# Optimization experiments

Hardware: AMD Instinct MI355X
Metric: run time of the kernel (lower is better)

Reference implementation:

```python
import jax, jax.numpy as jnp
import numpy as np

D_MODEL, D_K, D_FF, N = 1024, 128, 4096, 8192

def _linear_params(key, fan_in, fan_out):
    # mimic torch nn.Linear default init (uniform +/- 1/sqrt(fan_in))
    k1, k2 = jax.random.split(key)
    bound = 1.0 / np.sqrt(fan_in)
    W = jax.random.uniform(k1, (fan_out, fan_in), jnp.float32, -bound, bound)
    b = jax.random.uniform(k2, (fan_out,), jnp.float32, -bound, bound)
    return W, b

def setup_inputs() -> dict:
    key = jax.random.key(0)
    ks = jax.random.split(key, 7)
    x = jax.random.normal(ks[0], (N, D_MODEL), jnp.float32)
    Wq, bq = _linear_params(ks[1], D_MODEL, D_K)
    Wk, bk = _linear_params(ks[2], D_MODEL, D_K)
    Wv, bv = _linear_params(ks[3], D_MODEL, D_K)
    Wp, bp = _linear_params(ks[4], D_K, D_MODEL)
    W1, b1 = _linear_params(ks[5], D_MODEL, D_FF)
    W2, b2 = _linear_params(ks[6], D_FF, D_MODEL)
    return {"x": x, "Wq": Wq, "bq": bq, "Wk": Wk, "bk": bk, "Wv": Wv, "bv": bv,
            "Wp": Wp, "bp": bp, "W1": W1, "b1": b1, "W2": W2, "b2": b2}

def reference(x, Wq, bq, Wk, bk, Wv, bv, Wp, bp, W1, b1, W2, b2):
    # projections (torch Linear: x @ W.T + b)
    Q = x @ Wq.T + bq            # [n, d_k]
    K = x @ Wk.T + bk            # [n, d_k]
    V = x @ Wv.T + bv            # [n, d_k]
    # linear attention, original evaluation order: (Q @ K^T) @ V
    attn = Q @ K.T               # [n, n]
    context = attn @ V           # [n, d_k]
    out = context @ Wp.T + bp    # [n, d_model]
    x = x + out                  # residual 1
    h = jax.nn.relu(x @ W1.T + b1)  # [n, d_ff]
    return x + (h @ W2.T + b2)   # residual 2
```

## Files before the change

kernel.cpp:

```cpp
#include <hip/hip_runtime.h>


#define MROWS 8192
#define DMODEL 1024
#define DK 128
#define DFF 4096

typedef __attribute__((ext_vector_type(8))) __bf16 bf16x8;
typedef __attribute__((ext_vector_type(4))) float f32x4;

#define BAR()     __builtin_amdgcn_s_barrier()
#define WAITV(n)  asm volatile("s_waitcnt vmcnt(" #n ")" ::: "memory")
#define LGKMC(n)  asm volatile("s_waitcnt lgkmcnt(" #n ")" ::: "memory")
#define SCHED0()  __builtin_amdgcn_sched_barrier(0)
#define GLOAD(src, dst) __builtin_amdgcn_global_load_lds( \
    (const __attribute__((address_space(1))) void*)(src), \
    (__attribute__((address_space(3))) void*)(dst), 16, 0, 0)

#define LDSO(p) ((unsigned)(unsigned long long) \
    (__attribute__((address_space(3))) const char*)(const char*)(p))

__device__ __forceinline__ bf16x8 ldsr(unsigned off) {
    bf16x8 r;
    asm volatile("ds_read_b128 %0, %1" : "=v"(r) : "v"(off));
    return r;
}

__global__ __launch_bounds__(256) void cast_f32_bf16(
    const float* __restrict__ src, __bf16* __restrict__ dst, int n8)
{
    for (int i = blockIdx.x * blockDim.x + threadIdx.x; i < n8;
         i += gridDim.x * blockDim.x) {
        const float4 a = reinterpret_cast<const float4*>(src)[2 * i];
        const float4 b = reinterpret_cast<const float4*>(src)[2 * i + 1];
        bf16x8 o;
        o[0] = (__bf16)a.x; o[1] = (__bf16)a.y; o[2] = (__bf16)a.z; o[3] = (__bf16)a.w;
        o[4] = (__bf16)b.x; o[5] = (__bf16)b.y; o[6] = (__bf16)b.z; o[7] = (__bf16)b.w;
        reinterpret_cast<bf16x8*>(dst)[i] = o;
    }
}

__device__ __forceinline__ void cast_one(const float* s, __bf16* d, int i) {
    const float4 a = reinterpret_cast<const float4*>(s)[2 * i];
    const float4 b = reinterpret_cast<const float4*>(s)[2 * i + 1];
    bf16x8 o;
    o[0] = (__bf16)a.x; o[1] = (__bf16)a.y; o[2] = (__bf16)a.z; o[3] = (__bf16)a.w;
    o[4] = (__bf16)b.x; o[5] = (__bf16)b.y; o[6] = (__bf16)b.z; o[7] = (__bf16)b.w;
    reinterpret_cast<bf16x8*>(d)[i] = o;
}

__global__ __launch_bounds__(256) void cast6(
    const float* __restrict__ s0, __bf16* __restrict__ d0,
    const float* __restrict__ s1, __bf16* __restrict__ d1,
    const float* __restrict__ s2, __bf16* __restrict__ d2,
    const float* __restrict__ s3, __bf16* __restrict__ d3,
    const float* __restrict__ s4, __bf16* __restrict__ d4,
    const float* __restrict__ s5, __bf16* __restrict__ d5)
{
    const int b = blockIdx.x, t = threadIdx.x;
    if      (b <  64)  cast_one(s0, d0, b * 256 + t);
    else if (b < 128)  cast_one(s1, d1, (b - 64) * 256 + t);
    else if (b < 192)  cast_one(s2, d2, (b - 128) * 256 + t);
    else if (b < 256)  cast_one(s3, d3, (b - 192) * 256 + t);
    else if (b < 2304) cast_one(s4, d4, (b - 256) * 256 + t);
    else               cast_one(s5, d5, (b - 2304) * 256 + t);
}

__global__ void pack_bias3(const float* __restrict__ a, const float* __restrict__ b,
                           const float* __restrict__ c, float* __restrict__ o)
{
    const int t = threadIdx.x;
    o[t] = a[t]; o[128 + t] = b[t]; o[256 + t] = c[t];
}

__global__ __launch_bounds__(256) void ffn2_reduce(
    float* __restrict__ y, const __bf16* __restrict__ P0,
    const __bf16* __restrict__ P1, const float* __restrict__ b2, int n8)
{
    for (int i = blockIdx.x * blockDim.x + threadIdx.x; i < n8;
         i += gridDim.x * blockDim.x) {
        const int col0 = (i << 3) & (DMODEL - 1);
        const float4 ba = *reinterpret_cast<const float4*>(&b2[col0]);
        const float4 bb = *reinterpret_cast<const float4*>(&b2[col0 + 4]);
        float4 o0 = reinterpret_cast<const float4*>(y)[2 * i];
        float4 o1 = reinterpret_cast<const float4*>(y)[2 * i + 1];
        const bf16x8 p0 = reinterpret_cast<const bf16x8*>(P0)[i];
        const bf16x8 p1 = reinterpret_cast<const bf16x8*>(P1)[i];
        o0.x += (float)p0[0] + (float)p1[0] + ba.x;
        o0.y += (float)p0[1] + (float)p1[1] + ba.y;
        o0.z += (float)p0[2] + (float)p1[2] + ba.z;
        o0.w += (float)p0[3] + (float)p1[3] + ba.w;
        o1.x += (float)p0[4] + (float)p1[4] + bb.x;
        o1.y += (float)p0[5] + (float)p1[5] + bb.y;
        o1.z += (float)p0[6] + (float)p1[6] + bb.z;
        o1.w += (float)p0[7] + (float)p1[7] + bb.w;
        reinterpret_cast<float4*>(y)[2 * i]     = o0;
        reinterpret_cast<float4*>(y)[2 * i + 1] = o1;
    }
}

template<bool RELU, bool RESID, bool BIAS, bool OUTBF, bool DUAL>
__global__ __launch_bounds__(256) void gemm128(
    const __bf16* __restrict__ A, int lda,
    const __bf16* __restrict__ W,
    const float* __restrict__ bias,
    const float* __restrict__ resid,
    void* __restrict__ Cout, __bf16* __restrict__ Cbf, int ldc, int K)
{
    constexpr int BK = 32;
    __shared__ __bf16 As[128 * BK];
    __shared__ __bf16 Bs[128 * BK];

    const int tid  = threadIdx.x;
    const int lane = tid & 63;
    const int w    = tid >> 6;
    const int wm   = w >> 1;
    const int wn   = w & 1;
    const int fr   = lane & 15;
    const int fq   = lane >> 4;

    const long row0 = (long)blockIdx.y * 128;
    const long col0 = (long)blockIdx.x * 128;

    const int sr = (w << 4) + (lane >> 2);
    const int sc = (lane & 3) << 3;

    const __bf16* gA0 = A + (row0 + sr) * (long)lda + sc;
    const __bf16* gA1 = A + (row0 + 64 + sr) * (long)lda + sc;
    const __bf16* gW0 = W + (col0 + sr) * (long)K + sc;
    const __bf16* gW1 = W + (col0 + 64 + sr) * (long)K + sc;

    __bf16* lA0 = &As[(w << 4) * BK];
    __bf16* lA1 = &As[((w << 4) + 64) * BK];
    __bf16* lB0 = &Bs[(w << 4) * BK];
    __bf16* lB1 = &Bs[((w << 4) + 64) * BK];

    f32x4 acc[4][4] = {};

    for (int k0 = 0; k0 < K; k0 += BK) {
        GLOAD(gA0 + k0, lA0);
        GLOAD(gA1 + k0, lA1);
        GLOAD(gW0 + k0, lB0);
        GLOAD(gW1 + k0, lB1);
        __syncthreads();

        bf16x8 af[4], bfr[4];
        #pragma unroll
        for (int m = 0; m < 4; m++)
            af[m] = *reinterpret_cast<const bf16x8*>(
                &As[(wm * 64 + m * 16 + fr) * BK + fq * 8]);
        #pragma unroll
        for (int n = 0; n < 4; n++)
            bfr[n] = *reinterpret_cast<const bf16x8*>(
                &Bs[(wn * 64 + n * 16 + fr) * BK + fq * 8]);

        #pragma unroll
        for (int m = 0; m < 4; m++)
            #pragma unroll
            for (int n = 0; n < 4; n++)
                acc[m][n] = __builtin_amdgcn_mfma_f32_16x16x32_bf16(
                    af[m], bfr[n], acc[m][n], 0, 0, 0);
        __syncthreads();
    }

    float bc[4];
    #pragma unroll
    for (int n = 0; n < 4; n++)
        bc[n] = BIAS ? bias[col0 + wn * 64 + n * 16 + fr] : 0.0f;
    #pragma unroll
    for (int m = 0; m < 4; m++) {
        #pragma unroll
        for (int j = 0; j < 4; j++) {
            const long r = row0 + wm * 64 + m * 16 + fq * 4 + j;
            #pragma unroll
            for (int n = 0; n < 4; n++) {
                const long c = col0 + wn * 64 + n * 16 + fr;
                float v = acc[m][n][j] + bc[n];
                if constexpr (RESID) v += resid[r * ldc + c];
                if constexpr (RELU)  v = fmaxf(v, 0.0f);
                if constexpr (OUTBF) ((__bf16*)Cout)[r * ldc + c] = (__bf16)v;
                else                 ((float*)Cout)[r * ldc + c] = v;
                if constexpr (DUAL)  Cbf[r * ldc + c] = (__bf16)v;
            }
        }
    }
}

#define RD_B()                                             \
    _Pragma("unroll")                                      \
    for (int n = 0; n < 4; n++) {                          \
        bb[n][0] = ldsr(pB + rb0 + n * 2048);              \
        bb[n][1] = ldsr(pB + rb1 + n * 2048);              \
    }
#define RD_A(m0_, cnt_)                                    \
    _Pragma("unroll")                                      \
    for (int m = m0_; m < m0_ + cnt_; m++) {               \
        a[m][0] = ldsr(pA + rb0 + m * 2048);               \
        a[m][1] = ldsr(pA + rb1 + m * 2048);               \
    }
#define MFMA2(m0_)                                                            \
    _Pragma("unroll")                                                         \
    for (int m = m0_; m < m0_ + 2; m++)                                       \
        _Pragma("unroll")                                                     \
        for (int n = 0; n < 4; n++) {                                         \
            acc[m][n] = __builtin_amdgcn_mfma_f32_16x16x32_bf16(              \
                a[m][0], bb[n][0], acc[m][n], 0, 0, 0);                       \
            acc[m][n] = __builtin_amdgcn_mfma_f32_16x16x32_bf16(              \
                a[m][1], bb[n][1], acc[m][n], 0, 0, 0);                       \
        }

template<bool RELU, bool BIAS>
__global__ __launch_bounds__(512, 2) void gemm256p(
    const __bf16* __restrict__ A, int lda,
    const __bf16* __restrict__ W, int ldw,
    const float* __restrict__ bias,
    __bf16* __restrict__ Cout, long sstride, int ldc,
    int klen, int nb, int nbx)
{
    __shared__ char lds[8][16384];

    const int bid = blockIdx.x;
    const int sid = bid / nb;
    const int ib  = bid % nb;
    const int chunk = nb >> 3;
    const int swz   = (ib & 7) * chunk + (ib >> 3);
    const int bx    = swz % nbx;
    const int by    = swz / nbx;

    const long row0 = (long)by * 256;
    const long col0 = (long)bx * 256;

    const __bf16* Ash = A + (long)sid * klen;
    const __bf16* Wsh = W + (long)sid * klen;

    const int tid  = threadIdx.x;
    const int lane = tid & 63;
    const int w    = tid >> 6;
    const int wm   = w >> 2;
    const int wn   = w & 3;
    const int fr   = lane & 15;
    const int fq   = lane >> 4;

    const int srow8 = lane >> 3;
    const int scole = ((lane & 7) ^ srow8) << 3;
    const __bf16* gA = Ash + (row0 + w * 8 + srow8) * (long)lda + scole;
    const __bf16* gB = Wsh + (col0 + w * 8 + srow8) * (long)ldw + scole;

    char* ldsc = &lds[0][0];
    const unsigned lbase = LDSO(ldsc);
    const int nt = klen >> 6;

    auto stage = [&](int u, int j) {
        if (u >= nt) return;
        char* dst = ldsc + (((u & 1) << 2 | j) << 14) + (w << 10);
        if (j < 2) {
            const __bf16* s = gB + ((long)j * 128) * (long)ldw + (long)u * 64;
            GLOAD(s, dst);
            GLOAD(s + 64 * (long)ldw, dst + 8192);
        } else {
            const __bf16* s = gA + ((long)(j - 2) * 128) * (long)lda + (long)u * 64;
            GLOAD(s, dst);
            GLOAD(s + 64 * (long)lda, dst + 8192);
        }
    };

    const unsigned rb0 = fr * 128 + ((fq * 16) ^ ((fr & 7) << 4));
    const unsigned rb1 = fr * 128 + ((64 + fq * 16) ^ ((fr & 7) << 4));

    f32x4 acc[8][4] = {};
    bf16x8 a[8][2], bb[4][2];

    stage(0, 0); stage(0, 1); stage(0, 2); stage(0, 3);
    stage(1, 0); stage(1, 1); stage(1, 2); stage(1, 3);
    WAITV(8);
    BAR();

    for (int t = 0; t < nt; ++t) {
        const unsigned base = lbase + ((t & 1) << 16);
        const unsigned pB = base + ((wn >> 1) << 14) + ((wn & 1) << 13);
        const unsigned pA = base + ((2 + wm) << 14);

        RD_B();
        RD_A(0, 8);

        LGKMC(12); SCHED0();
        __builtin_amdgcn_s_setprio(1); MFMA2(0); __builtin_amdgcn_s_setprio(0);
        LGKMC(8); SCHED0();
        __builtin_amdgcn_s_setprio(1); MFMA2(2); __builtin_amdgcn_s_setprio(0);
        LGKMC(4); SCHED0();
        __builtin_amdgcn_s_setprio(1); MFMA2(4); __builtin_amdgcn_s_setprio(0);
        LGKMC(0); SCHED0();
        BAR();
        stage(t + 2, 0); stage(t + 2, 1);
        stage(t + 2, 2); stage(t + 2, 3);
        SCHED0();
        __builtin_amdgcn_s_setprio(1); MFMA2(6); __builtin_amdgcn_s_setprio(0);
        if (t + 2 < nt)      { WAITV(8); }
        else if (t + 1 < nt) { WAITV(0); }
        BAR();
    }

    __bf16* Cb = Cout + (long)sid * sstride;
    float bc[4];
    #pragma unroll
    for (int n = 0; n < 4; n++)
        bc[n] = BIAS ? bias[col0 + wn * 64 + n * 16 + fr] : 0.0f;

    __bf16* sw = reinterpret_cast<__bf16*>(ldsc) + (w << 13);
    #pragma unroll
    for (int m = 0; m < 8; m++)
        #pragma unroll
        for (int j = 0; j < 4; j++) {
            const int row = m * 16 + fq * 4 + j;
            #pragma unroll
            for (int n = 0; n < 4; n++) {
                float v = acc[m][n][j] + bc[n];
                if constexpr (RELU) v = fmaxf(v, 0.0f);
                sw[row * 64 + n * 16 + fr] = (__bf16)v;
            }
        }
    const long crow0 = row0 + wm * 128;
    const long ccol0 = col0 + wn * 64;
    #pragma unroll
    for (int i = 0; i < 16; i++) {
        const bf16x8 vv = *reinterpret_cast<const bf16x8*>(sw + i * 512 + lane * 8);
        const int r  = i * 8 + (lane >> 3);
        const int cg = (lane & 7) << 3;
        *reinterpret_cast<bf16x8*>(&Cb[(crow0 + r) * (long)ldc + ccol0 + cg]) = vv;
    }
}

__global__ __launch_bounds__(256) void ktv_partial(
    const __bf16* __restrict__ Kp, const __bf16* __restrict__ Vp,
    int ld, float* __restrict__ part)
{
    __shared__ float ks[32][DK];
    __shared__ float vs[32][DK];
    const int tid = threadIdx.x;
    const int ti  = tid >> 4;
    const int tj  = tid & 15;
    float acc[8][8] = {};
    const long base = (long)blockIdx.x * 128;

    for (int n0 = 0; n0 < 128; n0 += 32) {
        for (int t = tid; t < 512; t += 256) {
            const int r  = t >> 4;
            const int cc = (t & 15) << 3;
            const bf16x8 k8 = *reinterpret_cast<const bf16x8*>(
                &Kp[(base + n0 + r) * (long)ld + cc]);
            const bf16x8 v8 = *reinterpret_cast<const bf16x8*>(
                &Vp[(base + n0 + r) * (long)ld + cc]);
            #pragma unroll
            for (int u = 0; u < 8; u++) {
                ks[r][cc + u] = (float)k8[u];
                vs[r][cc + u] = (float)v8[u];
            }
        }
        __syncthreads();
        for (int n = 0; n < 32; n++) {
            float kk[8], vv[8];
            #pragma unroll
            for (int i = 0; i < 8; i++) kk[i] = ks[n][(ti << 3) + i];
            #pragma unroll
            for (int j = 0; j < 8; j++) vv[j] = vs[n][(tj << 3) + j];
            #pragma unroll
            for (int i = 0; i < 8; i++)
                #pragma unroll
                for (int j = 0; j < 8; j++)
                    acc[i][j] = fmaf(kk[i], vv[j], acc[i][j]);
        }
        __syncthreads();
    }

    float* dst = &part[(long)blockIdx.x * (DK * DK)];
    #pragma unroll
    for (int i = 0; i < 8; i++) {
        const int ig = (ti << 3) + i;
        *reinterpret_cast<float4*>(&dst[ig * DK + (tj << 3)]) =
            make_float4(acc[i][0], acc[i][1], acc[i][2], acc[i][3]);
        *reinterpret_cast<float4*>(&dst[ig * DK + (tj << 3) + 4]) =
            make_float4(acc[i][4], acc[i][5], acc[i][6], acc[i][7]);
    }
}

__global__ __launch_bounds__(256) void ktv_reduce(
    const float* __restrict__ part, __bf16* __restrict__ ktvT)
{
    const int t = blockIdx.x * 256 + threadIdx.x;
    const int i = t >> 7;
    const int j = t & 127;
    float s = 0.0f;
    for (int b = 0; b < 64; b++) s += part[(long)b * (DK * DK) + t];
    ktvT[j * DK + i] = (__bf16)s;
}

extern "C" void kernel_launch(void* const* d_in, const int* in_sizes, int n_in,
                              void* d_out, int out_size, void* d_ws, size_t ws_size,
                              hipStream_t stream) {
    const float* x  = (const float*)d_in[0];
    const float* Wq = (const float*)d_in[1];
    const float* bq = (const float*)d_in[2];
    const float* Wk = (const float*)d_in[3];
    const float* bk = (const float*)d_in[4];
    const float* Wv = (const float*)d_in[5];
    const float* bv = (const float*)d_in[6];
    const float* Wp = (const float*)d_in[7];
    const float* bp = (const float*)d_in[8];
    const float* W1 = (const float*)d_in[9];
    const float* b1 = (const float*)d_in[10];
    const float* W2 = (const float*)d_in[11];
    const float* b2 = (const float*)d_in[12];
    float* out = (float*)d_out;

    char* ws = (char*)d_ws;
    const size_t MB = 1ull << 20;
    __bf16* xb    = (__bf16*)(ws);
    __bf16* P0    = (__bf16*)(ws);
    __bf16* P1    = P0 + (long)MROWS * DMODEL;
    __bf16* x2b   = (__bf16*)(ws +  34 * MB);
    __bf16* Hb    = (__bf16*)(ws +  51 * MB);
    __bf16* QKVb  = (__bf16*)(ws + 119 * MB);
    __bf16* W1b   = (__bf16*)(ws + 126 * MB);
    __bf16* W2b   = (__bf16*)(ws + 135 * MB);
    __bf16* Wqkvb = (__bf16*)(ws + 144 * MB);
    __bf16* Wpb   = (__bf16*)(ws + 145 * MB);
    float*  Part  = (float*) (ws + 146 * MB);
    __bf16* KtvTb = (__bf16*)(ws + 151 * MB);
    __bf16* Ctxb  = (__bf16*)(ws + 152 * MB);
    float*  bqkvf = (float*) (ws + 155 * MB);

    const dim3 blk(256);

    cast_f32_bf16<<<2048, blk, 0, stream>>>(x, xb, MROWS * DMODEL / 8);
    cast6<<<4352, blk, 0, stream>>>(
        Wq, Wqkvb, Wk, Wqkvb + DK * DMODEL, Wv, Wqkvb + 2 * DK * DMODEL,
        Wp, Wpb, W1, W1b, W2, W2b);
    pack_bias3<<<1, 128, 0, stream>>>(bq, bk, bv, bqkvf);

    gemm128<false,false,true,true,false><<<dim3(3, 64), blk, 0, stream>>>(
        xb, DMODEL, Wqkvb, bqkvf, nullptr, QKVb, nullptr, 3 * DK, DMODEL);

    ktv_partial<<<64, blk, 0, stream>>>(QKVb + DK, QKVb + 2 * DK, 3 * DK, Part);
    ktv_reduce <<<64, blk, 0, stream>>>(Part, KtvTb);

    gemm128<false,false,false,true,false><<<dim3(1, 64), blk, 0, stream>>>(
        QKVb, 3 * DK, KtvTb, nullptr, nullptr, Ctxb, nullptr, DK, DK);

    gemm128<false,true,true,false,true><<<dim3(8, 64), blk, 0, stream>>>(
        Ctxb, DK, Wpb, bp, x, out, x2b, DMODEL, DK);

    gemm256p<true,true><<<512, 512, 0, stream>>>(
        x2b, DMODEL, W1b, DMODEL, b1, Hb, 0, DFF, DMODEL, 512, DFF / 256);

    gemm256p<false,false><<<256, 512, 0, stream>>>(
        Hb, DFF, W2b, DFF, nullptr, P0,
        (long)MROWS * DMODEL, DMODEL, DFF / 2, 128, DMODEL / 256);

    ffn2_reduce<<<2048, blk, 0, stream>>>(out, P0, P1, b2, MROWS * DMODEL / 8);
}
```

Before: 238.9 us.

## Software-pipeline LDS fragment reads across K tiles in gemm256p main loop

The gemm256p main loop is unrolled by two with explicit register ping-pong sets. The B fragments and the first two A fragments for the next K tile are read from LDS after the second barrier, so they overlap with the last MFMA cluster of the current tile. The goal is to hide LDS read latency at the start of each tile. In exchange it uses more VGPRs, which may spill under launch_bounds(512,2), and it assumes nt is even. The host buffers P0/P1 are renamed to P0b/P1b so they do not clash with the new register arrays.

```diff
diff --git a/kernel.cpp b/kernel.cpp
--- a/kernel.cpp
+++ b/kernel.cpp
@@ -186,28 +186,60 @@
     }
 }
 
-#define RD_B()                                             \
-    _Pragma("unroll")                                      \
-    for (int n = 0; n < 4; n++) {                          \
-        bb[n][0] = ldsr(pB + rb0 + n * 2048);              \
-        bb[n][1] = ldsr(pB + rb1 + n * 2048);              \
-    }
-#define RD_A(m0_, cnt_)                                    \
-    _Pragma("unroll")                                      \
-    for (int m = m0_; m < m0_ + cnt_; m++) {               \
-        a[m][0] = ldsr(pA + rb0 + m * 2048);               \
-        a[m][1] = ldsr(pA + rb1 + m * 2048);               \
-    }
-#define MFMA2(m0_)                                                            \
-    _Pragma("unroll")                                                         \
-    for (int m = m0_; m < m0_ + 2; m++)                                       \
-        _Pragma("unroll")                                                     \
-        for (int n = 0; n < 4; n++) {                                         \
-            acc[m][n] = __builtin_amdgcn_mfma_f32_16x16x32_bf16(              \
-                a[m][0], bb[n][0], acc[m][n], 0, 0, 0);                       \
-            acc[m][n] = __builtin_amdgcn_mfma_f32_16x16x32_bf16(              \
-                a[m][1], bb[n][1], acc[m][n], 0, 0, 0);                       \
-        }
+#define MF(va, vb, c) __builtin_amdgcn_mfma_f32_16x16x32_bf16(va, vb, c, 0, 0, 0)
+
+#define RD2(pr, pbase, idx)                              \
+    pr[0] = ldsr((pbase) + rb0 + (idx) * 2048);          \
+    pr[1] = ldsr((pbase) + rb1 + (idx) * 2048);
+
+#define CL(ma, mb, A0_, A1_, B0_, B1_, B2_, B3_)         \
+    __builtin_amdgcn_s_setprio(1);                       \
+    acc[ma][0] = MF(A0_[0], B0_[0], acc[ma][0]);         \
+    acc[ma][1] = MF(A0_[0], B1_[0], acc[ma][1]);         \
+    acc[ma][2] = MF(A0_[0], B2_[0], acc[ma][2]);         \
+    acc[ma][3] = MF(A0_[0], B3_[0], acc[ma][3]);         \
+    acc[mb][0] = MF(A1_[0], B0_[0], acc[mb][0]);         \
+    acc[mb][1] = MF(A1_[0], B1_[0], acc[mb][1]);         \
+    acc[mb][2] = MF(A1_[0], B2_[0], acc[mb][2]);         \
+    acc[mb][3] = MF(A1_[0], B3_[0], acc[mb][3]);         \
+    acc[ma][0] = MF(A0_[1], B0_[1], acc[ma][0]);         \
+    acc[ma][1] = MF(A0_[1], B1_[1], acc[ma][1]);         \
+    acc[ma][2] = MF(A0_[1], B2_[1], acc[ma][2]);         \
+    acc[ma][3] = MF(A0_[1], B3_[1], acc[ma][3]);         \
+    acc[mb][0] = MF(A1_[1], B0_[1], acc[mb][0]);         \
+    acc[mb][1] = MF(A1_[1], B1_[1], acc[mb][1]);         \
+    acc[mb][2] = MF(A1_[1], B2_[1], acc[mb][2]);         \
+    acc[mb][3] = MF(A1_[1], B3_[1], acc[mb][3]);         \
+    __builtin_amdgcn_s_setprio(0);
+
+#define TILE_BODY(t_, pA_, pBn_, pAn_, GUARD_,                                 \
+                  A2s, A3s, A4s, A5s, Bc0, Bc1, Bc2, Bc3, Bn0, Bn1, Bn2, Bn3)  \
+  {                                                                            \
+    RD2(A2s, pA_, 2); RD2(A3s, pA_, 3);                                        \
+    RD2(A4s, pA_, 4); RD2(A5s, pA_, 5);                                        \
+    RD2(Q6,  pA_, 6); RD2(Q7,  pA_, 7);                                        \
+    SCHED0();                                                                  \
+    LGKMC(12); SCHED0();                                                       \
+    CL(0, 1, Q4, Q5, Bc0, Bc1, Bc2, Bc3)                                       \
+    LGKMC(8); SCHED0();                                                        \
+    CL(2, 3, A2s, A3s, Bc0, Bc1, Bc2, Bc3)                                     \
+    LGKMC(4); SCHED0();                                                        \
+    CL(4, 5, A4s, A5s, Bc0, Bc1, Bc2, Bc3)                                     \
+    LGKMC(0); SCHED0();                                                        \
+    BAR();                                                                     \
+    stage((t_) + 2, 0); stage((t_) + 2, 1);                                    \
+    stage((t_) + 2, 2); stage((t_) + 2, 3);                                    \
+    if ((t_) + 2 < nt)      { WAITV(8); }                                      \
+    else if ((t_) + 1 < nt) { WAITV(0); }                                      \
+    BAR();                                                                     \
+    if (GUARD_) {                                                              \
+        RD2(Bn0, pBn_, 0); RD2(Bn1, pBn_, 1);                                  \
+        RD2(Bn2, pBn_, 2); RD2(Bn3, pBn_, 3);                                  \
+        RD2(Q4, pAn_, 0); RD2(Q5, pAn_, 1);                                    \
+    }                                                                          \
+    SCHED0();                                                                  \
+    CL(6, 7, Q6, Q7, Bc0, Bc1, Bc2, Bc3)                                       \
+  }
 
 template<bool RELU, bool BIAS>
 __global__ __launch_bounds__(512, 2) void gemm256p(
@@ -267,37 +299,28 @@
     const unsigned rb0 = fr * 128 + ((fq * 16) ^ ((fr & 7) << 4));
     const unsigned rb1 = fr * 128 + ((64 + fq * 16) ^ ((fr & 7) << 4));
 
+    const unsigned pB_e = lbase + ((wn >> 1) << 14) + ((wn & 1) << 13);
+    const unsigned pA_e = lbase + ((2 + wm) << 14);
+    const unsigned pB_o = pB_e + (1u << 16);
+    const unsigned pA_o = pA_e + (1u << 16);
+
     f32x4 acc[8][4] = {};
-    bf16x8 a[8][2], bb[4][2];
+    bf16x8 P0[2], P1[2], P2[2], P3[2];
+    bf16x8 Q0[2], Q1[2], Q2[2], Q3[2], Q4[2], Q5[2], Q6[2], Q7[2];
 
     stage(0, 0); stage(0, 1); stage(0, 2); stage(0, 3);
     stage(1, 0); stage(1, 1); stage(1, 2); stage(1, 3);
     WAITV(8);
     BAR();
-
-    for (int t = 0; t < nt; ++t) {
-        const unsigned base = lbase + ((t & 1) << 16);
-        const unsigned pB = base + ((wn >> 1) << 14) + ((wn & 1) << 13);
-        const unsigned pA = base + ((2 + wm) << 14);
-
-        RD_B();
-        RD_A(0, 8);
-
-        LGKMC(12); SCHED0();
-        __builtin_amdgcn_s_setprio(1); MFMA2(0); __builtin_amdgcn_s_setprio(0);
-        LGKMC(8); SCHED0();
-        __builtin_amdgcn_s_setprio(1); MFMA2(2); __builtin_amdgcn_s_setprio(0);
-        LGKMC(4); SCHED0();
-        __builtin_amdgcn_s_setprio(1); MFMA2(4); __builtin_amdgcn_s_setprio(0);
-        LGKMC(0); SCHED0();
-        BAR();
-        stage(t + 2, 0); stage(t + 2, 1);
-        stage(t + 2, 2); stage(t + 2, 3);
-        SCHED0();
-        __builtin_amdgcn_s_setprio(1); MFMA2(6); __builtin_amdgcn_s_setprio(0);
-        if (t + 2 < nt)      { WAITV(8); }
-        else if (t + 1 < nt) { WAITV(0); }
-        BAR();
+    RD2(P0, pB_e, 0); RD2(P1, pB_e, 1); RD2(P2, pB_e, 2); RD2(P3, pB_e, 3);
+    RD2(Q4, pA_e, 0); RD2(Q5, pA_e, 1);
+    SCHED0();
+
+    for (int tt = 0; tt < nt; tt += 2) {
+        TILE_BODY(tt, pA_e, pB_o, pA_o, 1,
+                  Q0, Q1, Q2, Q3, P0, P1, P2, P3, Q0, Q1, Q2, Q3)
+        TILE_BODY(tt + 1, pA_o, pB_e, pA_e, (tt + 2 < nt),
+                  P0, P1, P2, P3, Q0, Q1, Q2, Q3, P0, P1, P2, P3)
     }
 
     __bf16* Cb = Cout + (long)sid * sstride;
@@ -415,8 +438,8 @@
     char* ws = (char*)d_ws;
     const size_t MB = 1ull << 20;
     __bf16* xb    = (__bf16*)(ws);
-    __bf16* P0    = (__bf16*)(ws);
-    __bf16* P1    = P0 + (long)MROWS * DMODEL;
+    __bf16* P0b   = (__bf16*)(ws);
+    __bf16* P1b   = P0b + (long)MROWS * DMODEL;
     __bf16* x2b   = (__bf16*)(ws +  34 * MB);
     __bf16* Hb    = (__bf16*)(ws +  51 * MB);
     __bf16* QKVb  = (__bf16*)(ws + 119 * MB);
@@ -453,8 +476,8 @@
         x2b, DMODEL, W1b, DMODEL, b1, Hb, 0, DFF, DMODEL, 512, DFF / 256);
 
     gemm256p<false,false><<<256, 512, 0, stream>>>(
-        Hb, DFF, W2b, DFF, nullptr, P0,
+        Hb, DFF, W2b, DFF, nullptr, P0b,
         (long)MROWS * DMODEL, DMODEL, DFF / 2, 128, DMODEL / 256);
 
-    ffn2_reduce<<<2048, blk, 0, stream>>>(out, P0, P1, b2, MROWS * DMODEL / 8);
-}
+    ffn2_reduce<<<2048, blk, 0, stream>>>(out, P0b, P1b, b2, MROWS * DMODEL / 8);
+}
```

New measurement: 401.9 us. +68.2%, slower.

## Replace FFN 256x256 pipelined GEMM with 256x128 single-buffer GEMM

Applied to the files above, without the earlier changes.

Changes the FFN GEMM tile from 256x256 with 8 waves to 256x128 with 4 waves, doubling the grid and shrinking LDS per block to 48KB. This should let more blocks co-reside per CU. The double-buffered prefetch is removed, so each iteration loads, waits for all loads, then computes. The epilogue is split into two halves to fit the smaller LDS. The risk is exposed global-load latency and lower data reuse per tile.

```diff
diff --git a/kernel.cpp b/kernel.cpp
--- a/kernel.cpp
+++ b/kernel.cpp
@@ -210,14 +210,14 @@
         }
 
 template<bool RELU, bool BIAS>
-__global__ __launch_bounds__(512, 2) void gemm256p(
+__global__ __launch_bounds__(256, 2) void gemm256x128(
     const __bf16* __restrict__ A, int lda,
     const __bf16* __restrict__ W, int ldw,
     const float* __restrict__ bias,
     __bf16* __restrict__ Cout, long sstride, int ldc,
     int klen, int nb, int nbx)
 {
-    __shared__ char lds[8][16384];
+    __shared__ char lds[49152];
 
     const int bid = blockIdx.x;
     const int sid = bid / nb;
@@ -228,7 +228,7 @@
     const int by    = swz / nbx;
 
     const long row0 = (long)by * 256;
-    const long col0 = (long)bx * 256;
+    const long col0 = (long)bx * 128;
 
     const __bf16* Ash = A + (long)sid * klen;
     const __bf16* Wsh = W + (long)sid * klen;
@@ -236,49 +236,42 @@
     const int tid  = threadIdx.x;
     const int lane = tid & 63;
     const int w    = tid >> 6;
-    const int wm   = w >> 2;
-    const int wn   = w & 3;
+    const int wm   = w >> 1;
+    const int wn   = w & 1;
     const int fr   = lane & 15;
     const int fq   = lane >> 4;
 
-    const int srow8 = lane >> 3;
-    const int scole = ((lane & 7) ^ srow8) << 3;
-    const __bf16* gA = Ash + (row0 + w * 8 + srow8) * (long)lda + scole;
-    const __bf16* gB = Wsh + (col0 + w * 8 + srow8) * (long)ldw + scole;
-
-    char* ldsc = &lds[0][0];
+    const int scole = ((lane & 7) ^ (lane >> 3)) << 3;
+    const __bf16* gA = Ash + (row0 + w * 8 + (lane >> 3)) * (long)lda + scole;
+    const __bf16* gB = Wsh + (col0 + w * 8 + (lane >> 3)) * (long)ldw + scole;
+
+    char* ldsc = &lds[0];
     const unsigned lbase = LDSO(ldsc);
     const int nt = klen >> 6;
 
-    auto stage = [&](int u, int j) {
-        if (u >= nt) return;
-        char* dst = ldsc + (((u & 1) << 2 | j) << 14) + (w << 10);
-        if (j < 2) {
-            const __bf16* s = gB + ((long)j * 128) * (long)ldw + (long)u * 64;
-            GLOAD(s, dst);
-            GLOAD(s + 64 * (long)ldw, dst + 8192);
-        } else {
-            const __bf16* s = gA + ((long)(j - 2) * 128) * (long)lda + (long)u * 64;
-            GLOAD(s, dst);
-            GLOAD(s + 64 * (long)lda, dst + 8192);
-        }
+    auto stage = [&](int t) {
+        const __bf16* ap = gA + (long)t * 64;
+        const __bf16* bp = gB + (long)t * 64;
+        #pragma unroll
+        for (int r = 0; r < 8; r++)
+            GLOAD(ap + (long)(32 * r) * lda, ldsc + r * 4096 + (w << 10));
+        #pragma unroll
+        for (int r = 0; r < 4; r++)
+            GLOAD(bp + (long)(32 * r) * ldw, ldsc + 32768 + r * 4096 + (w << 10));
     };
 
     const unsigned rb0 = fr * 128 + ((fq * 16) ^ ((fr & 7) << 4));
     const unsigned rb1 = fr * 128 + ((64 + fq * 16) ^ ((fr & 7) << 4));
+    const unsigned pA = lbase + (wm << 14);
+    const unsigned pB = lbase + 32768 + (wn << 13);
 
     f32x4 acc[8][4] = {};
     bf16x8 a[8][2], bb[4][2];
 
-    stage(0, 0); stage(0, 1); stage(0, 2); stage(0, 3);
-    stage(1, 0); stage(1, 1); stage(1, 2); stage(1, 3);
-    WAITV(8);
-    BAR();
-
     for (int t = 0; t < nt; ++t) {
-        const unsigned base = lbase + ((t & 1) << 16);
-        const unsigned pB = base + ((wn >> 1) << 14) + ((wn & 1) << 13);
-        const unsigned pA = base + ((2 + wm) << 14);
+        stage(t);
+        WAITV(0);
+        BAR();
 
         RD_B();
         RD_A(0, 8);
@@ -290,13 +283,8 @@
         LGKMC(4); SCHED0();
         __builtin_amdgcn_s_setprio(1); MFMA2(4); __builtin_amdgcn_s_setprio(0);
         LGKMC(0); SCHED0();
-        BAR();
-        stage(t + 2, 0); stage(t + 2, 1);
-        stage(t + 2, 2); stage(t + 2, 3);
-        SCHED0();
         __builtin_amdgcn_s_setprio(1); MFMA2(6); __builtin_amdgcn_s_setprio(0);
-        if (t + 2 < nt)      { WAITV(8); }
-        else if (t + 1 < nt) { WAITV(0); }
+
         BAR();
     }
 
@@ -306,27 +294,31 @@
     for (int n = 0; n < 4; n++)
         bc[n] = BIAS ? bias[col0 + wn * 64 + n * 16 + fr] : 0.0f;
 
-    __bf16* sw = reinterpret_cast<__bf16*>(ldsc) + (w << 13);
-    #pragma unroll
-    for (int m = 0; m < 8; m++)
-        #pragma unroll
-        for (int j = 0; j < 4; j++) {
-            const int row = m * 16 + fq * 4 + j;
-            #pragma unroll
-            for (int n = 0; n < 4; n++) {
-                float v = acc[m][n][j] + bc[n];
-                if constexpr (RELU) v = fmaxf(v, 0.0f);
-                sw[row * 64 + n * 16 + fr] = (__bf16)v;
-            }
-        }
+    __bf16* sw = reinterpret_cast<__bf16*>(ldsc) + (w << 12);
     const long crow0 = row0 + wm * 128;
     const long ccol0 = col0 + wn * 64;
     #pragma unroll
-    for (int i = 0; i < 16; i++) {
-        const bf16x8 vv = *reinterpret_cast<const bf16x8*>(sw + i * 512 + lane * 8);
-        const int r  = i * 8 + (lane >> 3);
-        const int cg = (lane & 7) << 3;
-        *reinterpret_cast<bf16x8*>(&Cb[(crow0 + r) * (long)ldc + ccol0 + cg]) = vv;
+    for (int half = 0; half < 2; half++) {
+        #pragma unroll
+        for (int m = 0; m < 4; m++)
+            #pragma unroll
+            for (int j = 0; j < 4; j++) {
+                const int row = m * 16 + fq * 4 + j;
+                #pragma unroll
+                for (int n = 0; n < 4; n++) {
+                    float v = acc[half * 4 + m][n][j] + bc[n];
+                    if constexpr (RELU) v = fmaxf(v, 0.0f);
+                    sw[row * 64 + n * 16 + fr] = (__bf16)v;
+                }
+            }
+        #pragma unroll
+        for (int i = 0; i < 8; i++) {
+            const bf16x8 vv = *reinterpret_cast<const bf16x8*>(sw + i * 512 + lane * 8);
+            const int r  = half * 64 + i * 8 + (lane >> 3);
+            const int cg = (lane & 7) << 3;
+            *reinterpret_cast<bf16x8*>(&Cb[(crow0 + r) * (long)ldc + ccol0 + cg]) = vv;
+        }
+        __builtin_amdgcn_s_waitcnt(0);
     }
 }
 
@@ -415,8 +407,8 @@
     char* ws = (char*)d_ws;
     const size_t MB = 1ull << 20;
     __bf16* xb    = (__bf16*)(ws);
-    __bf16* P0    = (__bf16*)(ws);
-    __bf16* P1    = P0 + (long)MROWS * DMODEL;
+    __bf16* P0b   = (__bf16*)(ws);
+    __bf16* P1b   = P0b + (long)MROWS * DMODEL;
     __bf16* x2b   = (__bf16*)(ws +  34 * MB);
     __bf16* Hb    = (__bf16*)(ws +  51 * MB);
     __bf16* QKVb  = (__bf16*)(ws + 119 * MB);
@@ -449,12 +441,12 @@
     gemm128<false,true,true,false,true><<<dim3(8, 64), blk, 0, stream>>>(
         Ctxb, DK, Wpb, bp, x, out, x2b, DMODEL, DK);
 
-    gemm256p<true,true><<<512, 512, 0, stream>>>(
-        x2b, DMODEL, W1b, DMODEL, b1, Hb, 0, DFF, DMODEL, 512, DFF / 256);
-
-    gemm256p<false,false><<<256, 512, 0, stream>>>(
-        Hb, DFF, W2b, DFF, nullptr, P0,
-        (long)MROWS * DMODEL, DMODEL, DFF / 2, 128, DMODEL / 256);
-
-    ffn2_reduce<<<2048, blk, 0, stream>>>(out, P0, P1, b2, MROWS * DMODEL / 8);
-}
+    gemm256x128<true,true><<<1024, blk, 0, stream>>>(
+        x2b, DMODEL, W1b, DMODEL, b1, Hb, 0, DFF, DMODEL, 1024, DFF / 128);
+
+    gemm256x128<false,false><<<512, blk, 0, stream>>>(
+        Hb, DFF, W2b, DFF, nullptr, P0b,
+        (long)MROWS * DMODEL, DMODEL, DFF / 2, 256, DMODEL / 128);
+
+    ffn2_reduce<<<2048, blk, 0, stream>>>(out, P0b, P1b, b2, MROWS * DMODEL / 8);
+}
```

Measured after the change: 228.2 us. 4.5% less time.
